# Performance work log

Hardware: AMD Instinct MI355X
Metric: run time of the kernel (lower is better)

Reference implementation:

```python
import jax, jax.numpy as jnp
import numpy as np

N = 100000   # nodes
E = 1600000  # edges (before self-loops)
HIDDEN = 256
BN_EPS = 1e-5


def setup_inputs() -> dict:
    key = jax.random.key(0)
    ks = jax.random.split(key, 16)
    def lin(k, i, o):
        return jax.random.normal(k, (i, o), jnp.float32) / np.float32(np.sqrt(i))
    inp = {
        "x": jax.random.normal(ks[0], (N, 21), jnp.float32),
        "edge_index": jax.random.randint(ks[1], (2, E), 0, N),
        # GCNConv weights (stored [in, out]) + biases
        "W1": lin(ks[2], 21, HIDDEN), "b1": jnp.zeros((HIDDEN,), jnp.float32),
        "W2": lin(ks[3], HIDDEN, 112), "b2": jnp.zeros((112,), jnp.float32),
        # dense MLP
        "lin2_w": lin(ks[4], 112, 256), "lin2_b": jnp.zeros((256,), jnp.float32),
        "lin3_w": lin(ks[5], 256, 100), "lin3_b": jnp.zeros((100,), jnp.float32),
        "lin4_w": lin(ks[6], 100, 1),   "lin4_b": jnp.zeros((1,), jnp.float32),
        # batchnorm affine params
        "g1": jnp.ones((112,), jnp.float32), "be1": jnp.zeros((112,), jnp.float32),
        "g2": jnp.ones((256,), jnp.float32), "be2": jnp.zeros((256,), jnp.float32),
        "g3": jnp.ones((100,), jnp.float32), "be3": jnp.zeros((100,), jnp.float32),
    }
    return inp


def _gcn_conv(x, W, b, src, dst, n):
    # PyG GCNConv: h = xW; out_i = sum_j norm_ij * h_j (+ bias), sym-normalized w/ self-loops
    h = x @ W                                              # [N, C]
    deg = jax.ops.segment_sum(jnp.ones(src.shape, h.dtype), dst, num_segments=n)
    dinv = jnp.where(deg > 0, jax.lax.rsqrt(deg), 0.0)
    norm = dinv[src] * dinv[dst]                            # [E']
    out = jax.ops.segment_sum(h[src] * norm[:, None], dst, num_segments=n)
    return out + b


def _bn(x, g, b):
    # train-mode batchnorm: biased batch variance
    m = jnp.mean(x, axis=0)
    v = jnp.mean(jnp.square(x - m), axis=0)
    return (x - m) * jax.lax.rsqrt(v + BN_EPS) * g + b


def reference(x, edge_index, W1, b1, W2, b2, lin2_w, lin2_b, lin3_w, lin3_b,
              lin4_w, lin4_b, g1, be1, g2, be2, g3, be3):
    n = x.shape[0]
    loops = jnp.arange(n, dtype=edge_index.dtype)
    src = jnp.concatenate([edge_index[0], loops])
    dst = jnp.concatenate([edge_index[1], loops])
    h = jax.nn.relu(_gcn_conv(x, W1, b1, src, dst, n))
    h = _gcn_conv(h, W2, b2, src, dst, n)
    h = jax.nn.relu(_bn(h, g1, be1))
    # dropout: identity (eval / deterministic)
    h = jax.nn.relu(_bn(h @ lin2_w + lin2_b, g2, be2))
    h = jax.nn.relu(_bn(h @ lin3_w + lin3_b, g3, be3))
    return h @ lin4_w + lin4_b
```

## Files before the change

### kernel.cpp

```cpp
#include <hip/hip_runtime.h>

#define N_NODES 100000
#define N_EDGES 1600000

typedef _Float16 f16x8 __attribute__((ext_vector_type(8)));
typedef _Float16 f16x4 __attribute__((ext_vector_type(4)));
typedef _Float16 f16x2 __attribute__((ext_vector_type(2)));
typedef float fx4 __attribute__((ext_vector_type(4)));

#define NREP 16
#define NBUCK 196
#define CHUNK 8192
#define BCAP 12288

__global__ __launch_bounds__(256) void k_bin(const int* __restrict__ ei,
                                             unsigned* __restrict__ binned,
                                             int* __restrict__ gcount) {
  __shared__ unsigned pr[CHUNK];
  __shared__ unsigned srt[CHUNK];
  __shared__ unsigned char bk[CHUNK];
  __shared__ int hist[256], scanb[256], offs[256], bs[256], gb[256];
  const int t = threadIdx.x;
  const int e0 = blockIdx.x * CHUNK;
  const int n = min(CHUNK, N_EDGES - e0);
  hist[t] = 0;
  __syncthreads();
  for (int i = t; i < n; i += 256) {
    int src = ei[e0 + i], dst = ei[N_EDGES + e0 + i];
    int b = dst >> 9;
    pr[i] = ((unsigned)src << 9) | (unsigned)(dst & 511);
    bk[i] = (unsigned char)b;
    atomicAdd(&hist[b], 1);
  }
  __syncthreads();
  int v = hist[t];
  scanb[t] = v;
  __syncthreads();
  for (int off = 1; off < 256; off <<= 1) {
    int a = (t >= off) ? scanb[t - off] : 0;
    __syncthreads();
    scanb[t] += a;
    __syncthreads();
  }
  offs[t] = scanb[t] - v;
  bs[t] = scanb[t] - v;
  __syncthreads();
  for (int i = t; i < n; i += 256) {
    int b = bk[i];
    int p = atomicAdd(&offs[b], 1);
    srt[p] = pr[i];
  }
  if (t < NBUCK && v > 0) gb[t] = atomicAdd(&gcount[t], v);
  __syncthreads();
  int wave = t >> 6, lane = t & 63;
  for (int b = wave; b < NBUCK; b += 4) {
    int c = hist[b];
    if (c == 0) continue;
    int ls = bs[b], base = gb[b];
    unsigned* dstp = binned + (size_t)b * BCAP + base;
    for (int i = lane; i < c; i += 64) dstp[i] = srt[ls + i];
  }
}

__global__ void k_bscan(const int* __restrict__ gcount, int* __restrict__ gbase) {
  __shared__ int s[256];
  int t = threadIdx.x;
  int v = (t < NBUCK) ? gcount[t] : 0;
  s[t] = v;
  __syncthreads();
  for (int off = 1; off < 256; off <<= 1) {
    int a = (t >= off) ? s[t - off] : 0;
    __syncthreads();
    s[t] += a;
    __syncthreads();
  }
  if (t < NBUCK) gbase[t] = s[t] - v;
}

__global__ __launch_bounds__(256) void k_csr(const unsigned* __restrict__ binned,
                                             const int* __restrict__ gcount,
                                             const int* __restrict__ gbase,
                                             int* __restrict__ rowoff,
                                             int* __restrict__ cnt,
                                             float* __restrict__ dinv,
                                             int* __restrict__ csr) {
  __shared__ int hist[512], offs[512], ps[256];
  __shared__ unsigned srt[BCAP];
  const int b = blockIdx.x, t = threadIdx.x;
  const int n = min(gcount[b], BCAP);
  const int gb0 = gbase[b];
  const unsigned* bp = binned + (size_t)b * BCAP;
  hist[t] = 0;
  hist[t + 256] = 0;
  __syncthreads();
  for (int i = t; i < n; i += 256) atomicAdd(&hist[bp[i] & 511], 1);
  __syncthreads();
  int e0v = hist[2 * t], e1v = hist[2 * t + 1];
  ps[t] = e0v + e1v;
  __syncthreads();
  for (int off = 1; off < 256; off <<= 1) {
    int a = (t >= off) ? ps[t - off] : 0;
    __syncthreads();
    ps[t] += a;
    __syncthreads();
  }
  int excl = ps[t] - (e0v + e1v);
  offs[2 * t] = excl;
  offs[2 * t + 1] = excl + e0v;
  __syncthreads();
#pragma unroll
  for (int u = 0; u < 2; ++u) {
    int j = 2 * t + u;
    int nd = (b << 9) + j;
    if (nd < N_NODES) {
      int c = hist[j];
      cnt[nd] = c;
      dinv[nd] = rsqrtf((float)(c + 1));
      rowoff[nd] = gb0 + offs[j];
    }
  }
  __syncthreads();
  for (int i = t; i < n; i += 256) {
    unsigned p = bp[i];
    int d = p & 511;
    int pos = atomicAdd(&offs[d], 1);
    srt[pos] = p >> 9;
  }
  __syncthreads();
  for (int i = t; i < n; i += 256) csr[gb0 + i] = (int)srt[i];
}

__global__ void k_xpad(const float* __restrict__ x, const float* __restrict__ dinv,
                       float* __restrict__ xs) {
  int idx = blockIdx.x * 256 + threadIdx.x;
  if (idx >= N_NODES * 24) return;
  int r = idx / 24, c = idx - r * 24;
  xs[idx] = (c < 21) ? x[r * 21 + c] * dinv[r] : 0.f;
}

__global__ __launch_bounds__(256) void k_aggx(
    const float4* __restrict__ xs4, const float* __restrict__ dinv,
    const int* __restrict__ rowoff, const int* __restrict__ cnt,
    const int* __restrict__ csr, float4* __restrict__ aggx4) {
  int lane = threadIdx.x & 63, wave = threadIdx.x >> 6;
  int j = lane / 6, c4 = lane - j * 6;
  if (j >= 10) return;
  int i = blockIdx.x * 40 + wave * 10 + j;
  float di = dinv[i];
  int start = rowoff[i], len = cnt[i];
  float4 a0 = xs4[i * 6 + c4];
  float4 a1 = make_float4(0.f, 0.f, 0.f, 0.f);
  int e = 0;
  for (; e + 1 < len; e += 2) {
    int s0 = csr[start + e], s1 = csr[start + e + 1];
    float4 u0 = xs4[s0 * 6 + c4];
    float4 u1 = xs4[s1 * 6 + c4];
    a0.x += u0.x; a0.y += u0.y; a0.z += u0.z; a0.w += u0.w;
    a1.x += u1.x; a1.y += u1.y; a1.z += u1.z; a1.w += u1.w;
  }
  if (e < len) {
    int s0 = csr[start + e];
    float4 u0 = xs4[s0 * 6 + c4];
    a0.x += u0.x; a0.y += u0.y; a0.z += u0.z; a0.w += u0.w;
  }
  float4 r;
  r.x = di * (a0.x + a1.x); r.y = di * (a0.y + a1.y);
  r.z = di * (a0.z + a1.z); r.w = di * (a0.w + a1.w);
  aggx4[i * 6 + c4] = r;
}

__global__ __launch_bounds__(256) void k_gemm1(const float4* __restrict__ aggx4,
                                               const float* __restrict__ W1,
                                               const float* __restrict__ b1,
                                               _Float16* __restrict__ h1) {
  __shared__ float As[32][24];
  int t = threadIdx.x;
  int base = blockIdx.x * 32;
  for (int idx = t; idx < 32 * 6; idx += 256) {
    int m = idx / 6, q = idx - m * 6;
    *(float4*)(&As[m][q * 4]) = aggx4[(base + m) * 6 + q];
  }
  float w[21];
#pragma unroll
  for (int k = 0; k < 21; ++k) w[k] = W1[k * 256 + t];
  float bias = b1[t];
  __syncthreads();
  for (int m = 0; m < 32; ++m) {
    float acc = bias;
#pragma unroll
    for (int k = 0; k < 21; ++k) acc = fmaf(As[m][k], w[k], acc);
    h1[(size_t)(base + m) * 256 + t] = (_Float16)fmaxf(acc, 0.f);
  }
}

template <int K, int KPAD, int NOUT, int NR>
__global__ void k_wsplit(const float* __restrict__ W, _Float16* __restrict__ Wh,
                         _Float16* __restrict__ Wl) {
  int idx = blockIdx.x * 256 + threadIdx.x;
  if (idx >= NR * KPAD) return;
  int n = idx / KPAD, k = idx % KPAD;
  float v = (n < NOUT && k < K) ? W[k * NOUT + n] : 0.f;
  _Float16 h = (_Float16)v;
  Wh[idx] = h;
  Wl[idx] = (_Float16)(v - (float)h);
}

template <int K, int KPAD, int NT, int MT, int WR, int WC, int MINW,
          bool BN, bool STATS, bool F16IN, bool F16OUT>
__global__ __launch_bounds__(256, MINW) void k_mgemm(
    const void* __restrict__ Av, const _Float16* __restrict__ Wth,
    const _Float16* __restrict__ Wtl, const float* __restrict__ bias,
    const float* __restrict__ bn_a, const float* __restrict__ bn_c,
    const float* __restrict__ rowscale, void* __restrict__ Cv, int NOUTr,
    float* __restrict__ sums, float* __restrict__ sqs) {
  constexpr int BM = WR * MT * 16;
  constexpr int NR = WC * NT * 16;
  constexpr int BKP = 40;
  constexpr int ABYTES = BM * BKP * 2;
  constexpr int BBYTES = NR * BKP * 2;
  __shared__ __align__(16) char smem[ABYTES + 2 * BBYTES];
  _Float16* Ah = (_Float16*)smem;
  _Float16* Bh = (_Float16*)(smem + ABYTES);
  _Float16* Bl = (_Float16*)(smem + ABYTES + BBYTES);
  const float* A32 = (const float*)Av;
  const _Float16* A16 = (const _Float16*)Av;
  float* C = (float*)Cv;
  _Float16* C16 = (_Float16*)Cv;

  const int tid = threadIdx.x;
  const int lane = tid & 63, wave = tid >> 6;
  const int wr = wave % WR, wc = wave / WR;
  const int quad = lane >> 4, ln = lane & 15;
  const int rowbase = blockIdx.x * BM;

  fx4 acc[MT][NT];
#pragma unroll
  for (int mt = 0; mt < MT; ++mt)
#pragma unroll
    for (int j = 0; j < NT; ++j) acc[mt][j] = (fx4){0.f, 0.f, 0.f, 0.f};

  for (int kc = 0; kc < KPAD / 32; ++kc) {
    __syncthreads();
    for (int idx = tid; idx < BM * 4; idx += 256) {
      int m = idx >> 2, q = idx & 3;
      int gi = rowbase + m;
      int k = kc * 32 + q * 8;
      f16x8 hv;
#pragma unroll
      for (int t = 0; t < 8; ++t) hv[t] = (_Float16)0;
      if (gi < N_NODES && k < K) {
        if constexpr (F16IN) {
          hv = *(const f16x8*)(A16 + (size_t)gi * K + k);
          if constexpr (BN) {
            float4 a0 = *(const float4*)(bn_a + k);
            float4 a1 = *(const float4*)(bn_a + k + 4);
            float4 c0 = *(const float4*)(bn_c + k);
            float4 c1 = *(const float4*)(bn_c + k + 4);
            float av[8] = {a0.x, a0.y, a0.z, a0.w, a1.x, a1.y, a1.z, a1.w};
            float cv[8] = {c0.x, c0.y, c0.z, c0.w, c1.x, c1.y, c1.z, c1.w};
#pragma unroll
            for (int t = 0; t < 8; ++t)
              hv[t] = (_Float16)fmaxf(fmaf((float)hv[t], av[t], cv[t]), 0.f);
          }
        } else {
          float4 v0 = *(const float4*)(A32 + (size_t)gi * K + k);
          float4 v1 = *(const float4*)(A32 + (size_t)gi * K + k + 4);
          float vv[8] = {v0.x, v0.y, v0.z, v0.w, v1.x, v1.y, v1.z, v1.w};
          if constexpr (BN) {
            float4 a0 = *(const float4*)(bn_a + k);
            float4 a1 = *(const float4*)(bn_a + k + 4);
            float4 c0 = *(const float4*)(bn_c + k);
            float4 c1 = *(const float4*)(bn_c + k + 4);
            float av[8] = {a0.x, a0.y, a0.z, a0.w, a1.x, a1.y, a1.z, a1.w};
            float cv[8] = {c0.x, c0.y, c0.z, c0.w, c1.x, c1.y, c1.z, c1.w};
#pragma unroll
            for (int t = 0; t < 8; ++t)
              vv[t] = fmaxf(fmaf(vv[t], av[t], cv[t]), 0.f);
          }
#pragma unroll
          for (int t = 0; t < 8; ++t) hv[t] = (_Float16)vv[t];
        }
      }
      *(f16x8*)(Ah + m * BKP + q * 8) = hv;
    }
    for (int idx = tid; idx < NR * 4; idx += 256) {
      int n = idx >> 2, p = idx & 3;
      int src = n * KPAD + kc * 32 + p * 8;
      *(f16x8*)(Bh + n * BKP + p * 8) = *(const f16x8*)(Wth + src);
      *(f16x8*)(Bl + n * BKP + p * 8) = *(const f16x8*)(Wtl + src);
    }
    __syncthreads();
    f16x8 nf[MT];
#pragma unroll
    for (int mt = 0; mt < MT; ++mt) {
      int r = (wr * MT + mt) * 16 + ln;
      nf[mt] = *(const f16x8*)(Ah + r * BKP + quad * 8);
    }
#pragma unroll
    for (int j = 0; j < NT; ++j) {
      int n = (wc * NT + j) * 16 + ln;
      f16x8 wh = *(const f16x8*)(Bh + n * BKP + quad * 8);
      f16x8 wl = *(const f16x8*)(Bl + n * BKP + quad * 8);
#pragma unroll
      for (int mt = 0; mt < MT; ++mt)
        acc[mt][j] = __builtin_amdgcn_mfma_f32_16x16x32_f16(wh, nf[mt], acc[mt][j], 0, 0, 0);
#pragma unroll
      for (int mt = 0; mt < MT; ++mt)
        acc[mt][j] = __builtin_amdgcn_mfma_f32_16x16x32_f16(wl, nf[mt], acc[mt][j], 0, 0, 0);
    }
  }

  float* s_s = (float*)smem;
  float* s_q = s_s + NR;
  __syncthreads();
  if constexpr (STATS) {
    for (int c = tid; c < 2 * NR; c += 256) s_s[c] = 0.f;
    __syncthreads();
  }
  float rs[MT];
#pragma unroll
  for (int mt = 0; mt < MT; ++mt) {
    int nd = rowbase + (wr * MT + mt) * 16 + ln;
    rs[mt] = (rowscale != nullptr && nd < N_NODES) ? rowscale[nd] : 1.f;
  }
#pragma unroll
  for (int j = 0; j < NT; ++j) {
    int ch0 = (wc * NT + j) * 16 + quad * 4;
    bool cv = ch0 < NOUTr;
    float4 b4 = make_float4(0.f, 0.f, 0.f, 0.f);
    if (cv && bias != nullptr) b4 = *(const float4*)(bias + ch0);
    float sc[4] = {0.f, 0.f, 0.f, 0.f}, sq[4] = {0.f, 0.f, 0.f, 0.f};
#pragma unroll
    for (int mt = 0; mt < MT; ++mt) {
      int nd = rowbase + (wr * MT + mt) * 16 + ln;
      if (nd < N_NODES && cv) {
        float v0 = (acc[mt][j][0] + b4.x) * rs[mt];
        float v1 = (acc[mt][j][1] + b4.y) * rs[mt];
        float v2 = (acc[mt][j][2] + b4.z) * rs[mt];
        float v3 = (acc[mt][j][3] + b4.w) * rs[mt];
        if constexpr (F16OUT) {
          f16x4 o = {(_Float16)v0, (_Float16)v1, (_Float16)v2, (_Float16)v3};
          *(f16x4*)(C16 + (size_t)nd * NOUTr + ch0) = o;
        } else {
          float4 o = make_float4(v0, v1, v2, v3);
          *(float4*)(C + (size_t)nd * NOUTr + ch0) = o;
        }
        if constexpr (STATS) {
          sc[0] += v0; sq[0] = fmaf(v0, v0, sq[0]);
          sc[1] += v1; sq[1] = fmaf(v1, v1, sq[1]);
          sc[2] += v2; sq[2] = fmaf(v2, v2, sq[2]);
          sc[3] += v3; sq[3] = fmaf(v3, v3, sq[3]);
        }
      }
    }
    if constexpr (STATS) {
      if (cv) {
#pragma unroll
        for (int r = 0; r < 4; ++r) {
          float s = sc[r], q = sq[r];
          s += __shfl_xor(s, 1); q += __shfl_xor(q, 1);
          s += __shfl_xor(s, 2); q += __shfl_xor(q, 2);
          s += __shfl_xor(s, 4); q += __shfl_xor(q, 4);
          s += __shfl_xor(s, 8); q += __shfl_xor(q, 8);
          if (ln == 0) {
            atomicAdd(&s_s[ch0 + r], s);
            atomicAdd(&s_q[ch0 + r], q);
          }
        }
      }
    }
  }
  if constexpr (STATS) {
    __syncthreads();
    int rep = (blockIdx.x & (NREP - 1));
    for (int c = tid; c < NR; c += 256) {
      if (c < NOUTr) {
        atomicAdd(&sums[rep * NOUTr + c], s_s[c]);
        atomicAdd(&sqs[rep * NOUTr + c], s_q[c]);
      }
    }
  }
}

__global__ __launch_bounds__(256) void k_agg2(
    const f16x8* __restrict__ t2s8, const float* __restrict__ dinv,
    const int* __restrict__ rowoff, const int* __restrict__ cnt,
    const int* __restrict__ csr, const float* __restrict__ b2,
    float* __restrict__ g2) {
  int lane = threadIdx.x & 63, wave = threadIdx.x >> 6;
  int j = lane / 14, c = lane - j * 14;
  if (j >= 4) return;
  int i = blockIdx.x * 16 + wave * 4 + j;
  float di = dinv[i];
  int start = rowoff[i], len = cnt[i];
  f16x8 u = t2s8[i * 14 + c];
  fx4 a0, a1, b0, b1;
#pragma unroll
  for (int t = 0; t < 4; ++t) { a0[t] = (float)u[t]; b0[t] = (float)u[t + 4]; }
  a1 = (fx4){0.f, 0.f, 0.f, 0.f};
  b1 = (fx4){0.f, 0.f, 0.f, 0.f};
  int e = 0;
  for (; e + 1 < len; e += 2) {
    int s0 = csr[start + e], s1 = csr[start + e + 1];
    f16x8 u0 = t2s8[s0 * 14 + c];
    f16x8 u1 = t2s8[s1 * 14 + c];
#pragma unroll
    for (int t = 0; t < 4; ++t) {
      a0[t] += (float)u0[t]; b0[t] += (float)u0[t + 4];
      a1[t] += (float)u1[t]; b1[t] += (float)u1[t + 4];
    }
  }
  if (e < len) {
    int s0 = csr[start + e];
    f16x8 u0 = t2s8[s0 * 14 + c];
#pragma unroll
    for (int t = 0; t < 4; ++t) { a0[t] += (float)u0[t]; b0[t] += (float)u0[t + 4]; }
  }
  float4 blo = *(const float4*)(b2 + c * 8);
  float4 bhi = *(const float4*)(b2 + c * 8 + 4);
  float4 r0, r1;
  r0.x = fmaf(di, a0[0] + a1[0], blo.x); r0.y = fmaf(di, a0[1] + a1[1], blo.y);
  r0.z = fmaf(di, a0[2] + a1[2], blo.z); r0.w = fmaf(di, a0[3] + a1[3], blo.w);
  r1.x = fmaf(di, b0[0] + b1[0], bhi.x); r1.y = fmaf(di, b0[1] + b1[1], bhi.y);
  r1.z = fmaf(di, b0[2] + b1[2], bhi.z); r1.w = fmaf(di, b0[3] + b1[3], bhi.w);
  *(float4*)(g2 + (size_t)i * 112 + c * 8) = r0;
  *(float4*)(g2 + (size_t)i * 112 + c * 8 + 4) = r1;
}

template <int C>
__global__ void k_colstats(const float* __restrict__ X, float* __restrict__ sums,
                           float* __restrict__ sqs) {
  int c = threadIdx.x;
  if (c >= C) return;
  int chunk = (N_NODES + gridDim.x - 1) / gridDim.x;
  int i0 = blockIdx.x * chunk;
  int i1 = min(N_NODES, i0 + chunk);
  float s = 0.f, q = 0.f;
  for (int i = i0; i < i1; ++i) {
    float v = X[(size_t)i * C + c];
    s += v;
    q = fmaf(v, v, q);
  }
  int rep = (blockIdx.x & (NREP - 1));
  atomicAdd(&sums[rep * C + c], s);
  atomicAdd(&sqs[rep * C + c], q);
}

template <int C>
__global__ void k_bnfinal(const float* __restrict__ sums, const float* __restrict__ sqs,
                          const float* __restrict__ gamma, const float* __restrict__ beta,
                          float* __restrict__ bn_a, float* __restrict__ bn_c) {
  int c = threadIdx.x;
  if (c >= C) return;
  float s = 0.f, q = 0.f;
#pragma unroll
  for (int r = 0; r < NREP; ++r) {
    s += sums[r * C + c];
    q += sqs[r * C + c];
  }
  const float inv_n = 1.0f / (float)N_NODES;
  float mean = s * inv_n;
  float var = fmaxf(q * inv_n - mean * mean, 0.f);
  float rstd = 1.0f / sqrtf(var + 1e-5f);
  float a = gamma[c] * rstd;
  bn_a[c] = a;
  bn_c[c] = beta[c] - mean * a;
}

__global__ void k_final(const float* __restrict__ h4, const float* __restrict__ bn_a,
                        const float* __restrict__ bn_c, const float* __restrict__ w4,
                        const float* __restrict__ b4, float* __restrict__ out) {
  int lane = threadIdx.x & 63;
  int i = blockIdx.x * 4 + (threadIdx.x >> 6);
  float acc = fmaxf(fmaf(h4[(size_t)i * 100 + lane], bn_a[lane], bn_c[lane]), 0.f) * w4[lane];
  if (lane < 36) {
    int k = lane + 64;
    acc += fmaxf(fmaf(h4[(size_t)i * 100 + k], bn_a[k], bn_c[k]), 0.f) * w4[k];
  }
#pragma unroll
  for (int off = 32; off >= 1; off >>= 1) acc += __shfl_down(acc, off);
  if (lane == 0) out[i] = acc + b4[0];
}

extern "C" void kernel_launch(void* const* d_in, const int* in_sizes, int n_in,
                              void* d_out, int out_size, void* d_ws, size_t ws_size,
                              hipStream_t stream) {
  const float* x   = (const float*)d_in[0];
  const int*   ei  = (const int*)d_in[1];
  const float* W1  = (const float*)d_in[2];
  const float* b1  = (const float*)d_in[3];
  const float* W2  = (const float*)d_in[4];
  const float* b2  = (const float*)d_in[5];
  const float* l2w = (const float*)d_in[6];
  const float* l2b = (const float*)d_in[7];
  const float* l3w = (const float*)d_in[8];
  const float* l3b = (const float*)d_in[9];
  const float* l4w = (const float*)d_in[10];
  const float* l4b = (const float*)d_in[11];
  const float* g1  = (const float*)d_in[12];
  const float* be1 = (const float*)d_in[13];
  const float* g2w = (const float*)d_in[14];
  const float* be2 = (const float*)d_in[15];
  const float* g3  = (const float*)d_in[16];
  const float* be3 = (const float*)d_in[17];
  float* out = (float*)d_out;

  char* base = (char*)d_ws;
  size_t off = 0;
  auto alloc = [&](size_t bytes) -> char* {
    char* p = base + off;
    off = (off + bytes + 255) & ~(size_t)255;
    return p;
  };
  int*   cnt    = (int*)alloc((size_t)N_NODES * 4);
  int*   rowoff = (int*)alloc((size_t)N_NODES * 4);
  float* dinv   = (float*)alloc((size_t)N_NODES * 4);
  int*   csr    = (int*)alloc((size_t)N_EDGES * 4);
  unsigned* binned = (unsigned*)alloc((size_t)NBUCK * BCAP * 4);
  int*   gcount = (int*)alloc(NBUCK * 4);
  int*   gbase  = (int*)alloc(NBUCK * 4);
  float* stats  = (float*)alloc((size_t)NREP * 960 * 4);
  float* bnco   = (float*)alloc(960 * 4);
  float* xs     = (float*)alloc((size_t)N_NODES * 24 * 4);
  float* aggx   = (float*)alloc((size_t)N_NODES * 24 * 4);
  _Float16* h1  = (_Float16*)alloc((size_t)N_NODES * 256 * 2);
  _Float16* t2s = (_Float16*)alloc((size_t)N_NODES * 112 * 2);
  float* g2buf  = (float*)alloc((size_t)N_NODES * 112 * 4);
  _Float16* wt2h = (_Float16*)alloc(112 * 256 * 2);
  _Float16* wt2l = (_Float16*)alloc(112 * 256 * 2);
  _Float16* wt3h = (_Float16*)alloc(256 * 128 * 2);
  _Float16* wt3l = (_Float16*)alloc(256 * 128 * 2);
  _Float16* wt4h = (_Float16*)alloc(112 * 256 * 2);
  _Float16* wt4l = (_Float16*)alloc(112 * 256 * 2);
  float* h4 = g2buf;

  float* sums1 = stats;
  float* sqs1  = sums1 + NREP * 112;
  float* sums2 = sqs1 + NREP * 112;
  float* sqs2  = sums2 + NREP * 256;
  float* sums3 = sqs2 + NREP * 256;
  float* sqs3  = sums3 + NREP * 112;
  float* bn_a1 = bnco + 0,   *bn_c1 = bnco + 112;
  float* bn_a2 = bnco + 224, *bn_c2 = bnco + 480;
  float* bn_a3 = bnco + 736, *bn_c3 = bnco + 848;

  hipMemsetAsync(gcount, 0, NBUCK * 4, stream);
  hipMemsetAsync(stats, 0, (size_t)NREP * 960 * 4, stream);

  k_bin<<<NBUCK, 256, 0, stream>>>(ei, binned, gcount);
  k_bscan<<<1, 256, 0, stream>>>(gcount, gbase);
  k_csr<<<NBUCK, 256, 0, stream>>>(binned, gcount, gbase, rowoff, cnt, dinv, csr);

  k_wsplit<256, 256, 112, 112><<<112, 256, 0, stream>>>(W2, wt2h, wt2l);
  k_wsplit<112, 128, 256, 256><<<128, 256, 0, stream>>>(l2w, wt3h, wt3l);
  k_wsplit<256, 256, 100, 112><<<112, 256, 0, stream>>>(l3w, wt4h, wt4l);

  k_xpad<<<(N_NODES * 24 + 255) / 256, 256, 0, stream>>>(x, dinv, xs);
  k_aggx<<<2500, 256, 0, stream>>>((const float4*)xs, dinv, rowoff, cnt, csr,
                                   (float4*)aggx);
  k_gemm1<<<3125, 256, 0, stream>>>((const float4*)aggx, W1, b1, h1);

  k_mgemm<256, 256, 7, 2, 4, 1, 4, false, false, true, true><<<782, 256, 0, stream>>>(
      h1, wt2h, wt2l, nullptr, nullptr, nullptr, dinv, t2s, 112, nullptr, nullptr);
  k_agg2<<<6250, 256, 0, stream>>>((const f16x8*)t2s, dinv, rowoff, cnt, csr, b2,
                                   g2buf);

  k_colstats<112><<<1600, 128, 0, stream>>>(g2buf, sums1, sqs1);
  k_bnfinal<112><<<1, 128, 0, stream>>>(sums1, sqs1, g1, be1, bn_a1, bn_c1);

  k_mgemm<112, 128, 8, 2, 2, 2, 3, true, true, false, true><<<1563, 256, 0, stream>>>(
      g2buf, wt3h, wt3l, l2b, bn_a1, bn_c1, nullptr, h1, 256, sums2, sqs2);
  k_bnfinal<256><<<1, 256, 0, stream>>>(sums2, sqs2, g2w, be2, bn_a2, bn_c2);

  k_mgemm<256, 256, 7, 2, 4, 1, 4, true, true, true, false><<<782, 256, 0, stream>>>(
      h1, wt4h, wt4l, l3b, bn_a2, bn_c2, nullptr, h4, 100, sums3, sqs3);
  k_bnfinal<100><<<1, 128, 0, stream>>>(sums3, sqs3, g3, be3, bn_a3, bn_c3);

  k_final<<<25000, 256, 0, stream>>>(h4, bn_a3, bn_c3, l4w, l4b, out);
}
```

Measured before the change: 467.8 us.

## Drop split-fp16 weight correction, store aggregated features in fp16, prefetch A tiles

```diff
diff --git a/kernel.cpp b/kernel.cpp
--- a/kernel.cpp
+++ b/kernel.cpp
@@ -5,7 +5,6 @@
 
 typedef _Float16 f16x8 __attribute__((ext_vector_type(8)));
 typedef _Float16 f16x4 __attribute__((ext_vector_type(4)));
-typedef _Float16 f16x2 __attribute__((ext_vector_type(2)));
 typedef float fx4 __attribute__((ext_vector_type(4)));
 
 #define NREP 16
@@ -194,34 +193,32 @@
 }
 
 template <int K, int KPAD, int NOUT, int NR>
-__global__ void k_wsplit(const float* __restrict__ W, _Float16* __restrict__ Wh,
-                         _Float16* __restrict__ Wl) {
+__global__ void k_wcvt(const float* __restrict__ W, _Float16* __restrict__ Wh) {
   int idx = blockIdx.x * 256 + threadIdx.x;
   if (idx >= NR * KPAD) return;
   int n = idx / KPAD, k = idx % KPAD;
   float v = (n < NOUT && k < K) ? W[k * NOUT + n] : 0.f;
-  _Float16 h = (_Float16)v;
-  Wh[idx] = h;
-  Wl[idx] = (_Float16)(v - (float)h);
+  Wh[idx] = (_Float16)v;
 }
 
 template <int K, int KPAD, int NT, int MT, int WR, int WC, int MINW,
           bool BN, bool STATS, bool F16IN, bool F16OUT>
 __global__ __launch_bounds__(256, MINW) void k_mgemm(
-    const void* __restrict__ Av, const _Float16* __restrict__ Wth,
-    const _Float16* __restrict__ Wtl, const float* __restrict__ bias,
-    const float* __restrict__ bn_a, const float* __restrict__ bn_c,
-    const float* __restrict__ rowscale, void* __restrict__ Cv, int NOUTr,
-    float* __restrict__ sums, float* __restrict__ sqs) {
+    const void* __restrict__ Av, const _Float16* __restrict__ Wt,
+    const float* __restrict__ bias, const float* __restrict__ bn_a,
+    const float* __restrict__ bn_c, const float* __restrict__ rowscale,
+    void* __restrict__ Cv, int NOUTr, float* __restrict__ sums,
+    float* __restrict__ sqs) {
   constexpr int BM = WR * MT * 16;
   constexpr int NR = WC * NT * 16;
   constexpr int BKP = 40;
+  constexpr int NC = KPAD / 32;
+  constexpr int AIT = BM * 4 / 256;
   constexpr int ABYTES = BM * BKP * 2;
   constexpr int BBYTES = NR * BKP * 2;
-  __shared__ __align__(16) char smem[ABYTES + 2 * BBYTES];
+  __shared__ __align__(16) char smem[ABYTES + BBYTES];
   _Float16* Ah = (_Float16*)smem;
   _Float16* Bh = (_Float16*)(smem + ABYTES);
-  _Float16* Bl = (_Float16*)(smem + ABYTES + BBYTES);
   const float* A32 = (const float*)Av;
   const _Float16* A16 = (const _Float16*)Av;
   float* C = (float*)Cv;
@@ -239,57 +236,78 @@
 #pragma unroll
     for (int j = 0; j < NT; ++j) acc[mt][j] = (fx4){0.f, 0.f, 0.f, 0.f};
 
-  for (int kc = 0; kc < KPAD / 32; ++kc) {
-    __syncthreads();
-    for (int idx = tid; idx < BM * 4; idx += 256) {
+  f16x8 pf16[AIT];
+  fx4 pf32a[AIT], pf32b[AIT];
+
+  auto loadA = [&](int kc) {
+#pragma unroll
+    for (int it = 0; it < AIT; ++it) {
+      int idx = tid + it * 256;
       int m = idx >> 2, q = idx & 3;
       int gi = rowbase + m;
       int k = kc * 32 + q * 8;
-      f16x8 hv;
-#pragma unroll
-      for (int t = 0; t < 8; ++t) hv[t] = (_Float16)0;
-      if (gi < N_NODES && k < K) {
-        if constexpr (F16IN) {
-          hv = *(const f16x8*)(A16 + (size_t)gi * K + k);
-          if constexpr (BN) {
-            float4 a0 = *(const float4*)(bn_a + k);
-            float4 a1 = *(const float4*)(bn_a + k + 4);
-            float4 c0 = *(const float4*)(bn_c + k);
-            float4 c1 = *(const float4*)(bn_c + k + 4);
-            float av[8] = {a0.x, a0.y, a0.z, a0.w, a1.x, a1.y, a1.z, a1.w};
-            float cv[8] = {c0.x, c0.y, c0.z, c0.w, c1.x, c1.y, c1.z, c1.w};
-#pragma unroll
-            for (int t = 0; t < 8; ++t)
-              hv[t] = (_Float16)fmaxf(fmaf((float)hv[t], av[t], cv[t]), 0.f);
-          }
+      bool ok = (gi < N_NODES) && (k < K);
+      if constexpr (F16IN) {
+        f16x8 z;
+#pragma unroll
+        for (int t = 0; t < 8; ++t) z[t] = (_Float16)0;
+        pf16[it] = ok ? *(const f16x8*)(A16 + (size_t)gi * K + k) : z;
+      } else {
+        if (ok) {
+          pf32a[it] = *(const fx4*)(A32 + (size_t)gi * K + k);
+          pf32b[it] = *(const fx4*)(A32 + (size_t)gi * K + k + 4);
         } else {
-          float4 v0 = *(const float4*)(A32 + (size_t)gi * K + k);
-          float4 v1 = *(const float4*)(A32 + (size_t)gi * K + k + 4);
-          float vv[8] = {v0.x, v0.y, v0.z, v0.w, v1.x, v1.y, v1.z, v1.w};
-          if constexpr (BN) {
-            float4 a0 = *(const float4*)(bn_a + k);
-            float4 a1 = *(const float4*)(bn_a + k + 4);
-            float4 c0 = *(const float4*)(bn_c + k);
-            float4 c1 = *(const float4*)(bn_c + k + 4);
-            float av[8] = {a0.x, a0.y, a0.z, a0.w, a1.x, a1.y, a1.z, a1.w};
-            float cv[8] = {c0.x, c0.y, c0.z, c0.w, c1.x, c1.y, c1.z, c1.w};
-#pragma unroll
-            for (int t = 0; t < 8; ++t)
-              vv[t] = fmaxf(fmaf(vv[t], av[t], cv[t]), 0.f);
-          }
-#pragma unroll
-          for (int t = 0; t < 8; ++t) hv[t] = (_Float16)vv[t];
+          pf32a[it] = (fx4){0.f, 0.f, 0.f, 0.f};
+          pf32b[it] = (fx4){0.f, 0.f, 0.f, 0.f};
         }
       }
+    }
+  };
+
+  auto writeA = [&](int kc) {
+#pragma unroll
+    for (int it = 0; it < AIT; ++it) {
+      int idx = tid + it * 256;
+      int m = idx >> 2, q = idx & 3;
+      int k = kc * 32 + q * 8;
+      float vv[8];
+      if constexpr (F16IN) {
+#pragma unroll
+        for (int t = 0; t < 8; ++t) vv[t] = (float)pf16[it][t];
+      } else {
+#pragma unroll
+        for (int t = 0; t < 4; ++t) { vv[t] = pf32a[it][t]; vv[t + 4] = pf32b[it][t]; }
+      }
+      if constexpr (BN) {
+        if (k < K) {
+          float4 a0 = *(const float4*)(bn_a + k);
+          float4 a1 = *(const float4*)(bn_a + k + 4);
+          float4 c0 = *(const float4*)(bn_c + k);
+          float4 c1 = *(const float4*)(bn_c + k + 4);
+          float av[8] = {a0.x, a0.y, a0.z, a0.w, a1.x, a1.y, a1.z, a1.w};
+          float cv[8] = {c0.x, c0.y, c0.z, c0.w, c1.x, c1.y, c1.z, c1.w};
+#pragma unroll
+          for (int t = 0; t < 8; ++t) vv[t] = fmaxf(fmaf(vv[t], av[t], cv[t]), 0.f);
+        }
+      }
+      f16x8 hv;
+#pragma unroll
+      for (int t = 0; t < 8; ++t) hv[t] = (_Float16)vv[t];
       *(f16x8*)(Ah + m * BKP + q * 8) = hv;
     }
+  };
+
+  loadA(0);
+  for (int kc = 0; kc < NC; ++kc) {
+    __syncthreads();
+    writeA(kc);
     for (int idx = tid; idx < NR * 4; idx += 256) {
       int n = idx >> 2, p = idx & 3;
-      int src = n * KPAD + kc * 32 + p * 8;
-      *(f16x8*)(Bh + n * BKP + p * 8) = *(const f16x8*)(Wth + src);
-      *(f16x8*)(Bl + n * BKP + p * 8) = *(const f16x8*)(Wtl + src);
-    }
-    __syncthreads();
+      *(f16x8*)(Bh + n * BKP + p * 8) =
+          *(const f16x8*)(Wt + n * KPAD + kc * 32 + p * 8);
+    }
+    __syncthreads();
+    if (kc + 1 < NC) loadA(kc + 1);
     f16x8 nf[MT];
 #pragma unroll
     for (int mt = 0; mt < MT; ++mt) {
@@ -300,13 +318,9 @@
     for (int j = 0; j < NT; ++j) {
       int n = (wc * NT + j) * 16 + ln;
       f16x8 wh = *(const f16x8*)(Bh + n * BKP + quad * 8);
-      f16x8 wl = *(const f16x8*)(Bl + n * BKP + quad * 8);
 #pragma unroll
       for (int mt = 0; mt < MT; ++mt)
         acc[mt][j] = __builtin_amdgcn_mfma_f32_16x16x32_f16(wh, nf[mt], acc[mt][j], 0, 0, 0);
-#pragma unroll
-      for (int mt = 0; mt < MT; ++mt)
-        acc[mt][j] = __builtin_amdgcn_mfma_f32_16x16x32_f16(wl, nf[mt], acc[mt][j], 0, 0, 0);
     }
   }
 
@@ -386,7 +400,7 @@
     const f16x8* __restrict__ t2s8, const float* __restrict__ dinv,
     const int* __restrict__ rowoff, const int* __restrict__ cnt,
     const int* __restrict__ csr, const float* __restrict__ b2,
-    float* __restrict__ g2) {
+    _Float16* __restrict__ g2) {
   int lane = threadIdx.x & 63, wave = threadIdx.x >> 6;
   int j = lane / 14, c = lane - j * 14;
   if (j >= 4) return;
@@ -418,18 +432,21 @@
   }
   float4 blo = *(const float4*)(b2 + c * 8);
   float4 bhi = *(const float4*)(b2 + c * 8 + 4);
-  float4 r0, r1;
-  r0.x = fmaf(di, a0[0] + a1[0], blo.x); r0.y = fmaf(di, a0[1] + a1[1], blo.y);
-  r0.z = fmaf(di, a0[2] + a1[2], blo.z); r0.w = fmaf(di, a0[3] + a1[3], blo.w);
-  r1.x = fmaf(di, b0[0] + b1[0], bhi.x); r1.y = fmaf(di, b0[1] + b1[1], bhi.y);
-  r1.z = fmaf(di, b0[2] + b1[2], bhi.z); r1.w = fmaf(di, b0[3] + b1[3], bhi.w);
-  *(float4*)(g2 + (size_t)i * 112 + c * 8) = r0;
-  *(float4*)(g2 + (size_t)i * 112 + c * 8 + 4) = r1;
+  f16x8 o;
+  o[0] = (_Float16)fmaf(di, a0[0] + a1[0], blo.x);
+  o[1] = (_Float16)fmaf(di, a0[1] + a1[1], blo.y);
+  o[2] = (_Float16)fmaf(di, a0[2] + a1[2], blo.z);
+  o[3] = (_Float16)fmaf(di, a0[3] + a1[3], blo.w);
+  o[4] = (_Float16)fmaf(di, b0[0] + b1[0], bhi.x);
+  o[5] = (_Float16)fmaf(di, b0[1] + b1[1], bhi.y);
+  o[6] = (_Float16)fmaf(di, b0[2] + b1[2], bhi.z);
+  o[7] = (_Float16)fmaf(di, b0[3] + b1[3], bhi.w);
+  *(f16x8*)(g2 + (size_t)i * 112 + c * 8) = o;
 }
 
 template <int C>
-__global__ void k_colstats(const float* __restrict__ X, float* __restrict__ sums,
-                           float* __restrict__ sqs) {
+__global__ void k_colstats16(const _Float16* __restrict__ X, float* __restrict__ sums,
+                             float* __restrict__ sqs) {
   int c = threadIdx.x;
   if (c >= C) return;
   int chunk = (N_NODES + gridDim.x - 1) / gridDim.x;
@@ -437,7 +454,7 @@
   int i1 = min(N_NODES, i0 + chunk);
   float s = 0.f, q = 0.f;
   for (int i = i0; i < i1; ++i) {
-    float v = X[(size_t)i * C + c];
+    float v = (float)X[(size_t)i * C + c];
     s += v;
     q = fmaf(v, v, q);
   }
@@ -525,14 +542,11 @@
   float* aggx   = (float*)alloc((size_t)N_NODES * 24 * 4);
   _Float16* h1  = (_Float16*)alloc((size_t)N_NODES * 256 * 2);
   _Float16* t2s = (_Float16*)alloc((size_t)N_NODES * 112 * 2);
-  float* g2buf  = (float*)alloc((size_t)N_NODES * 112 * 4);
-  _Float16* wt2h = (_Float16*)alloc(112 * 256 * 2);
-  _Float16* wt2l = (_Float16*)alloc(112 * 256 * 2);
-  _Float16* wt3h = (_Float16*)alloc(256 * 128 * 2);
-  _Float16* wt3l = (_Float16*)alloc(256 * 128 * 2);
-  _Float16* wt4h = (_Float16*)alloc(112 * 256 * 2);
-  _Float16* wt4l = (_Float16*)alloc(112 * 256 * 2);
-  float* h4 = g2buf;
+  _Float16* g2h = (_Float16*)alloc((size_t)N_NODES * 112 * 2);
+  float* h4     = (float*)alloc((size_t)N_NODES * 112 * 4);
+  _Float16* wt2 = (_Float16*)alloc(112 * 256 * 2);
+  _Float16* wt3 = (_Float16*)alloc(256 * 128 * 2);
+  _Float16* wt4 = (_Float16*)alloc(112 * 256 * 2);
 
   float* sums1 = stats;
   float* sqs1  = sums1 + NREP * 112;
@@ -551,9 +565,9 @@
   k_bscan<<<1, 256, 0, stream>>>(gcount, gbase);
   k_csr<<<NBUCK, 256, 0, stream>>>(binned, gcount, gbase, rowoff, cnt, dinv, csr);
 
-  k_wsplit<256, 256, 112, 112><<<112, 256, 0, stream>>>(W2, wt2h, wt2l);
-  k_wsplit<112, 128, 256, 256><<<128, 256, 0, stream>>>(l2w, wt3h, wt3l);
-  k_wsplit<256, 256, 100, 112><<<112, 256, 0, stream>>>(l3w, wt4h, wt4l);
+  k_wcvt<256, 256, 112, 112><<<112, 256, 0, stream>>>(W2, wt2);
+  k_wcvt<112, 128, 256, 256><<<128, 256, 0, stream>>>(l2w, wt3);
+  k_wcvt<256, 256, 100, 112><<<112, 256, 0, stream>>>(l3w, wt4);
 
   k_xpad<<<(N_NODES * 24 + 255) / 256, 256, 0, stream>>>(x, dinv, xs);
   k_aggx<<<2500, 256, 0, stream>>>((const float4*)xs, dinv, rowoff, cnt, csr,
@@ -561,19 +575,19 @@
   k_gemm1<<<3125, 256, 0, stream>>>((const float4*)aggx, W1, b1, h1);
 
   k_mgemm<256, 256, 7, 2, 4, 1, 4, false, false, true, true><<<782, 256, 0, stream>>>(
-      h1, wt2h, wt2l, nullptr, nullptr, nullptr, dinv, t2s, 112, nullptr, nullptr);
+      h1, wt2, nullptr, nullptr, nullptr, dinv, t2s, 112, nullptr, nullptr);
   k_agg2<<<6250, 256, 0, stream>>>((const f16x8*)t2s, dinv, rowoff, cnt, csr, b2,
-                                   g2buf);
-
-  k_colstats<112><<<1600, 128, 0, stream>>>(g2buf, sums1, sqs1);
+                                   g2h);
+
+  k_colstats16<112><<<1600, 128, 0, stream>>>(g2h, sums1, sqs1);
   k_bnfinal<112><<<1, 128, 0, stream>>>(sums1, sqs1, g1, be1, bn_a1, bn_c1);
 
-  k_mgemm<112, 128, 8, 2, 2, 2, 3, true, true, false, true><<<1563, 256, 0, stream>>>(
-      g2buf, wt3h, wt3l, l2b, bn_a1, bn_c1, nullptr, h1, 256, sums2, sqs2);
+  k_mgemm<112, 128, 8, 2, 2, 2, 4, true, true, true, true><<<1563, 256, 0, stream>>>(
+      g2h, wt3, l2b, bn_a1, bn_c1, nullptr, h1, 256, sums2, sqs2);
   k_bnfinal<256><<<1, 256, 0, stream>>>(sums2, sqs2, g2w, be2, bn_a2, bn_c2);
 
   k_mgemm<256, 256, 7, 2, 4, 1, 4, true, true, true, false><<<782, 256, 0, stream>>>(
-      h1, wt4h, wt4l, l3b, bn_a2, bn_c2, nullptr, h4, 100, sums3, sqs3);
+      h1, wt4, l3b, bn_a2, bn_c2, nullptr, h4, 100, sums3, sqs3);
   k_bnfinal<100><<<1, 128, 0, stream>>>(sums3, sqs3, g3, be3, bn_a3, bn_c3);
 
   k_final<<<25000, 256, 0, stream>>>(h4, bn_a3, bn_c3, l4w, l4b, out);
```

New measurement: 435.1 us. -7.0%, faster.
